# Kernel tuning notes

Measured on AMD Instinct MI355X. Metric: run time of the kernel, lower is better.

## Reference

```python
import jax, jax.numpy as jnp
import numpy as np

B, N, F, G, H = 8, 1024, 512, 128, 8
D = F // H  # head_dim = 64


def setup_inputs() -> dict:
    key = jax.random.key(0)
    ks = jax.random.split(key, 24)
    def lin(k, fan_in, shape):
        return jax.random.normal(k, shape, jnp.float32) / np.sqrt(fan_in)
    return {
        "features": jax.random.normal(ks[0], (B, N, F), jnp.float32),
        "geometry": jax.random.normal(ks[1], (B, N, G), jnp.float32),
        "coords": jax.random.normal(ks[2], (B, N, 3), jnp.float32),
        # nnx.MultiHeadAttention params (q/k/v/out dense, with bias)
        "wq": lin(ks[3], F, (F, F)), "bq": jnp.zeros((F,), jnp.float32),
        "wk": lin(ks[4], F, (F, F)), "bk": jnp.zeros((F,), jnp.float32),
        "wv": lin(ks[5], F, (F, F)), "bv": jnp.zeros((F,), jnp.float32),
        "wo": lin(ks[6], F, (F, F)), "bo": jnp.zeros((F,), jnp.float32),
        # geometry q/k/v linears
        "gq_w": lin(ks[7], G, (G, F)), "gq_b": jnp.zeros((F,), jnp.float32),
        "gk_w": lin(ks[8], G, (G, F)), "gk_b": jnp.zeros((F,), jnp.float32),
        "gv_w": lin(ks[9], G, (G, F)), "gv_b": jnp.zeros((F,), jnp.float32),
        # distance MLP: Linear(1->H), gelu, Linear(H->H)
        "d1_w": lin(ks[10], 1, (1, H)), "d1_b": jnp.zeros((H,), jnp.float32),
        "d2_w": lin(ks[11], H, (H, H)), "d2_b": jnp.zeros((H,), jnp.float32),
        # output projection
        "op_w": lin(ks[12], F, (F, F)), "op_b": jnp.zeros((F,), jnp.float32),
    }


def _forward(features, geometry, coords,
             wq, bq, wk, bk, wv, bv, wo, bo,
             gq_w, gq_b, gk_w, gk_b, gv_w, gv_b,
             d1_w, d1_b, d2_w, d2_b, op_w, op_b):
    scale = jnp.sqrt(jnp.float32(D))
    # --- standard multi-head self-attention branch (nnx.MultiHeadAttention) ---
    q = (features @ wq + bq).reshape(B, N, H, D)
    k = (features @ wk + bk).reshape(B, N, H, D)
    v = (features @ wv + bv).reshape(B, N, H, D)
    scores = jnp.einsum("bqhd,bkhd->bhqk", q, k) / scale
    attn = jax.nn.softmax(scores, axis=-1)
    feat_att = jnp.einsum("bhqk,bkhd->bqhd", attn, v).reshape(B, N, F)
    feat_att = feat_att @ wo + bo
    # --- geometry attention branch ---
    gq = geometry @ gq_w + gq_b
    gk = geometry @ gk_w + gk_b
    gv = geometry @ gv_w + gv_b
    g_scores = jnp.einsum("bqd,bkd->bqk", gq, gk) / scale
    # pairwise distances (B,N,N,1); clamp for sqrt-at-zero safety (diagonal)
    diff = coords[:, :, None, :] - coords[:, None, :, :]
    dist = jnp.sqrt(jnp.maximum(jnp.sum(diff * diff, -1, keepdims=True), 1e-12))
    dw = jax.nn.gelu(dist @ d1_w + d1_b) @ d2_w + d2_b  # (B,N,N,H)
    # transpose to (B,H,N,N) then mean over heads == mean over last axis
    g_scores = g_scores + jnp.mean(dw, axis=-1)
    g_attn = jax.nn.softmax(g_scores, axis=-1)
    geom_att = jnp.einsum("bqk,bkd->bqd", g_attn, gv)
    return (feat_att + geom_att) @ op_w + op_b


def reference(features, geometry, coords,
              wq, bq, wk, bk, wv, bv, wo, bo,
              gq_w, gq_b, gk_w, gk_b, gv_w, gv_b,
              d1_w, d1_b, d2_w, d2_b, op_w, op_b):
    return _forward(features, geometry, coords,
                    wq, bq, wk, bk, wv, bv, wo, bo,
                    gq_w, gq_b, gk_w, gk_b, gv_w, gv_b,
                    d1_w, d1_b, d2_w, d2_b, op_w, op_b)
```

## Files before the change

kernel.cpp:

```cpp
#include <hip/hip_runtime.h>

typedef __bf16 bf16_t;
typedef __bf16 bf16x8 __attribute__((ext_vector_type(8)));
typedef __bf16 bf16x4v __attribute__((ext_vector_type(4)));
typedef float f32x4 __attribute__((ext_vector_type(4)));

#define MFMA16(a, b, c) __builtin_amdgcn_mfma_f32_16x16x32_bf16((a), (b), (c), 0, 0, 0)

static constexpr int B_ = 8, N_ = 1024, F_ = 512, H_ = 8;
static constexpr int M_ = B_ * N_;
static constexpr float LOG2E = 1.4426950408889634f;

__device__ __forceinline__ void gl_lds16(const bf16_t* gsrc, bf16_t* ldst) {
  __builtin_amdgcn_global_load_lds(
      (const __attribute__((address_space(1))) void*)gsrc,
      (__attribute__((address_space(3))) void*)ldst, 16, 0, 0);
}

__device__ __forceinline__ float gelu_tanh(float u) {
  float g = 0.7978845608028654f * fmaf(0.044715f * u * u, u, u);
  float e = __expf(2.f * g);
  float t = 1.f - 2.f / (e + 1.f);
  return 0.5f * u * (1.f + t);
}

struct PrepArgs {
  const float *features, *geometry;
  const float *wq, *wk, *wv, *wo, *op_w;
  const float *gq_w, *gk_w, *gv_w;
  const float *bq, *bk, *bv, *gq_b, *gv_b;
  const float *d1w, *d1b, *d2w, *d2b;
  bf16_t *featBF, *geomBF, *gkwBF, *WqkvT, *GqvT, *WoT, *OpT;
  float *bqkv, *gqvb, *dlut;
};

static constexpr int PR_C0 = 4096;
static constexpr int PR_C1 = PR_C0 + 1024;
static constexpr int PR_GKC = PR_C1 + 64;
static constexpr int PR_WQ = PR_GKC + 256;
static constexpr int PR_WK = PR_WQ + 256;
static constexpr int PR_WV = PR_WK + 256;
static constexpr int PR_WO = PR_WV + 256;
static constexpr int PR_OP = PR_WO + 256;
static constexpr int PR_GQ = PR_OP + 64;
static constexpr int PR_GV = PR_GQ + 64;
static constexpr int PR_B1 = PR_GV + 6;
static constexpr int PR_B2 = PR_B1 + 4;
static constexpr int PR_LUT = PR_B2 + 16;
static constexpr int PR_TOTAL = PR_LUT;

__device__ __forceinline__ void prep_cast(const float* __restrict__ in,
                                          bf16_t* __restrict__ out, int blk) {
  int i = blk * 256 + threadIdx.x;
  float4 v = ((const float4*)in)[i];
  bf16x4v o;
  o[0] = (bf16_t)v.x; o[1] = (bf16_t)v.y; o[2] = (bf16_t)v.z; o[3] = (bf16_t)v.w;
  ((bf16x4v*)out)[i] = o;
}

__device__ __forceinline__ void prep_transpose(const float* __restrict__ W,
                                               bf16_t* __restrict__ Wt,
                                               int K, int N, int ldo, int idx,
                                               float (*t)[33]) {
  const int bx = idx & 15, by = idx >> 4;
  const int kb = by * 32, cb = bx * 32;
  const int tx = threadIdx.x & 31, ty = threadIdx.x >> 5;
#pragma unroll
  for (int i = 0; i < 4; ++i)
    t[ty * 4 + i][tx] = W[(long)(kb + ty * 4 + i) * N + cb + tx];
  __syncthreads();
#pragma unroll
  for (int i = 0; i < 4; ++i)
    Wt[(long)(cb + ty * 4 + i) * ldo + kb + tx] = (bf16_t)t[tx][ty * 4 + i];
}

__global__ __launch_bounds__(256) void k_prep(PrepArgs p) {
  __shared__ float tsh[32][33];
  const int blk = blockIdx.x;
  if (blk < PR_C0) {
    prep_cast(p.features, p.featBF, blk);
  } else if (blk < PR_C1) {
    prep_cast(p.geometry, p.geomBF, blk - PR_C0);
  } else if (blk < PR_GKC) {
    prep_cast(p.gk_w, p.gkwBF, blk - PR_C1);
  } else if (blk < PR_WQ) {
    prep_transpose(p.wq, p.WqkvT, 512, 512, 512, blk - PR_GKC, tsh);
  } else if (blk < PR_WK) {
    prep_transpose(p.wk, p.WqkvT + 512 * 512, 512, 512, 512, blk - PR_WQ, tsh);
  } else if (blk < PR_WV) {
    prep_transpose(p.wv, p.WqkvT + 1024 * 512, 512, 512, 512, blk - PR_WK, tsh);
  } else if (blk < PR_WO) {
    prep_transpose(p.wo, p.WoT, 512, 512, 512, blk - PR_WV, tsh);
  } else if (blk < PR_OP) {
    prep_transpose(p.op_w, p.OpT, 512, 512, 512, blk - PR_WO, tsh);
  } else if (blk < PR_GQ) {
    prep_transpose(p.gq_w, p.GqvT, 128, 512, 128, blk - PR_OP, tsh);
  } else if (blk < PR_GV) {
    prep_transpose(p.gv_w, p.GqvT + 512 * 128, 128, 512, 128, blk - PR_GQ, tsh);
  } else if (blk < PR_B1) {
    int i = (blk - PR_GV) * 256 + threadIdx.x;
    p.bqkv[i] = i < 512 ? p.bq[i] : (i < 1024 ? p.bk[i - 512] : p.bv[i - 1024]);
  } else if (blk < PR_B2) {
    int i = (blk - PR_B1) * 256 + threadIdx.x;
    p.gqvb[i] = i < 512 ? p.gq_b[i] : p.gv_b[i - 512];
  } else {
    int i = (blk - PR_B2) * 256 + threadIdx.x;
    float d = (i + 0.5f) * (16.f / 4096.f);
    float s = 0.f;
#pragma unroll
    for (int h = 0; h < 8; ++h) s += p.d2b[h];
    s *= 0.125f;
#pragma unroll
    for (int j = 0; j < 8; ++j) {
      float w2 = 0.f;
#pragma unroll
      for (int h = 0; h < 8; ++h) w2 += p.d2w[j * 8 + h];
      s = fmaf(gelu_tanh(fmaf(d, p.d1w[j], p.d1b[j])), w2 * 0.125f, s);
    }
    p.dlut[i] = s;
  }
}

struct GemmArgs {
  const bf16_t* A; const bf16_t* Bt;
  const float* bias; const float* addSrc; const bf16_t* addSrcB;
  const float* coords; const float* lut;
  float* outF; bf16_t* outB;
  bf16_t* outT;
  int vtileFrom;
  long strideAb; long strideBb;
  int lda, ldb, K, ldout;
  float scale;
};

__device__ __forceinline__ void gemm128_core(const GemmArgs& g, int mBase, int cBase,
                                             bf16_t (*As)[64], bf16_t (*Bs)[64]) {
  const int tid = threadIdx.x;
  const int w = tid >> 6, lane = tid & 63;
  const int lr = lane & 15, lg = lane >> 4;
  const int wr = w >> 1, wc = w & 1;
  const int batch = mBase >> 10;

  const int srow = lane >> 3;
  const int scol = (lane & 7) * 8;
  const bf16_t* Ag = g.A + (long)batch * g.strideAb +
                     (long)((mBase & 1023) + w * 32 + srow) * g.lda + scol;
  const bf16_t* Bg = g.Bt + (long)batch * g.strideBb +
                     (long)(cBase + w * 32 + srow) * g.ldb + scol;
  bf16_t* Al = &As[w * 32][0];
  bf16_t* Bl = &Bs[w * 32][0];

  f32x4 zero = {0.f, 0.f, 0.f, 0.f};
  f32x4 acc[4][4];
#pragma unroll
  for (int i = 0; i < 4; ++i)
#pragma unroll
    for (int j = 0; j < 4; ++j) acc[i][j] = zero;

  for (int k0 = 0; k0 < g.K; k0 += 64) {
#pragma unroll
    for (int is = 0; is < 4; ++is) {
      gl_lds16(Ag + (long)(is * 8) * g.lda + k0, Al + is * 8 * 64);
      gl_lds16(Bg + (long)(is * 8) * g.ldb + k0, Bl + is * 8 * 64);
    }
    __syncthreads();
#pragma unroll
    for (int ks = 0; ks < 2; ++ks) {
      bf16x8 a[4], b[4];
#pragma unroll
      for (int i = 0; i < 4; ++i) {
        a[i] = *(const bf16x8*)(&As[wr * 64 + i * 16 + lr][ks * 32 + lg * 8]);
        b[i] = *(const bf16x8*)(&Bs[wc * 64 + i * 16 + lr][ks * 32 + lg * 8]);
      }
#pragma unroll
      for (int mf = 0; mf < 4; ++mf)
#pragma unroll
        for (int nf = 0; nf < 4; ++nf)
          acc[mf][nf] = MFMA16(a[mf], b[nf], acc[mf][nf]);
    }
    __syncthreads();
  }

  const int c0 = cBase + wc * 64;
  float bias4[4];
#pragma unroll
  for (int nf = 0; nf < 4; ++nf)
    bias4[nf] = g.bias ? g.bias[c0 + nf * 16 + lr] : 0.f;
  const bool vtile = (g.outT != nullptr) && (cBase >= g.vtileFrom);
#pragma unroll
  for (int mf = 0; mf < 4; ++mf) {
    const int r0 = mBase + wr * 64 + mf * 16 + lg * 4;
    const int r0b = r0 & 1023;
#pragma unroll
    for (int nf = 0; nf < 4; ++nf) {
      const int c = c0 + nf * 16 + lr;
      if (vtile) {
        bf16x4v vv;
#pragma unroll
        for (int rg = 0; rg < 4; ++rg)
          vv[rg] = (bf16_t)(acc[mf][nf][rg] * g.scale + bias4[nf]);
        *(bf16x4v*)(&g.outT[((long)batch * 512 + (c - g.vtileFrom)) * 1024 + r0b]) = vv;
      } else {
#pragma unroll
        for (int rg = 0; rg < 4; ++rg) {
          const int r = r0 + rg;
          float v = acc[mf][nf][rg] * g.scale + bias4[nf];
          if (g.addSrc) v += g.addSrc[(long)r * g.ldout + c];
          const long oi = (long)r * g.ldout + c;
          if (g.outF) g.outF[oi] = v;
          if (g.outB) g.outB[oi] = (bf16_t)v;
        }
      }
    }
  }
}

__global__ __launch_bounds__(256) void k_gemm128_dual(GemmArgs g1, GemmArgs g2) {
  __shared__ alignas(16) bf16_t As[128][64];
  __shared__ alignas(16) bf16_t Bs[128][64];
  const int bx = blockIdx.x;
  if (bx < 768) {
    gemm128_core(g1, (bx / 12) * 128, (bx % 12) * 128, As, Bs);
  } else {
    const int i = bx - 768;
    gemm128_core(g2, (i / 8) * 128, (i % 8) * 128, As, Bs);
  }
}

__device__ __forceinline__ void gemm128_dist(const GemmArgs& g, int mBase, int cBase,
                                             char* smemc) {
  bf16_t (*As)[64] = (bf16_t (*)[64])smemc;
  bf16_t (*Bs)[64] = (bf16_t (*)[64])(smemc + 16384);
  bf16_t* Lut = (bf16_t*)(smemc + 32768);
  const int tid = threadIdx.x;
  const int w = tid >> 6, lane = tid & 63;
  const int lr = lane & 15, lg = lane >> 4;
  const int wr = w >> 1, wc = w & 1;
  const int batch = mBase >> 10;

  {
    const float4* src = (const float4*)g.lut;
#pragma unroll
    for (int i = 0; i < 4; ++i) {
      float4 v = src[tid + i * 256];
      bf16x4v o;
      o[0] = (bf16_t)(v.x * LOG2E); o[1] = (bf16_t)(v.y * LOG2E);
      o[2] = (bf16_t)(v.z * LOG2E); o[3] = (bf16_t)(v.w * LOG2E);
      ((bf16x4v*)Lut)[tid + i * 256] = o;
    }
  }

  const int srow = lane >> 3;
  const int scol = (lane & 7) * 8;
  const bf16_t* Ag = g.A + (long)batch * g.strideAb +
                     (long)((mBase & 1023) + w * 32 + srow) * g.lda + scol;
  const bf16_t* Bg = g.Bt + (long)batch * g.strideBb +
                     (long)(cBase + w * 32 + srow) * g.ldb + scol;
  bf16_t* Al = &As[w * 32][0];
  bf16_t* Bl = &Bs[w * 32][0];

  f32x4 zero = {0.f, 0.f, 0.f, 0.f};
  f32x4 acc[4][4];
#pragma unroll
  for (int i = 0; i < 4; ++i)
#pragma unroll
    for (int j = 0; j < 4; ++j) acc[i][j] = zero;

  for (int k0 = 0; k0 < g.K; k0 += 64) {
#pragma unroll
    for (int is = 0; is < 4; ++is) {
      gl_lds16(Ag + (long)(is * 8) * g.lda + k0, Al + is * 8 * 64);
      gl_lds16(Bg + (long)(is * 8) * g.ldb + k0, Bl + is * 8 * 64);
    }
    __syncthreads();
#pragma unroll
    for (int ks = 0; ks < 2; ++ks) {
      bf16x8 a[4], b[4];
#pragma unroll
      for (int i = 0; i < 4; ++i) {
        a[i] = *(const bf16x8*)(&As[wr * 64 + i * 16 + lr][ks * 32 + lg * 8]);
        b[i] = *(const bf16x8*)(&Bs[wc * 64 + i * 16 + lr][ks * 32 + lg * 8]);
      }
#pragma unroll
      for (int mf = 0; mf < 4; ++mf)
#pragma unroll
        for (int nf = 0; nf < 4; ++nf)
          acc[mf][nf] = MFMA16(a[mf], b[nf], acc[mf][nf]);
    }
    __syncthreads();
  }

  const int c0 = cBase + wc * 64;
  float ckx[4], cky[4], ckz[4];
#pragma unroll
  for (int nf = 0; nf < 4; ++nf) {
    const float* ck = g.coords + ((long)batch * 1024 + c0 + nf * 16 + lr) * 3;
    ckx[nf] = ck[0]; cky[nf] = ck[1]; ckz[nf] = ck[2];
  }
#pragma unroll
  for (int mf = 0; mf < 4; ++mf) {
    const int r0 = mBase + wr * 64 + mf * 16 + lg * 4;
    float cqx[4], cqy[4], cqz[4];
#pragma unroll
    for (int rg = 0; rg < 4; ++rg) {
      const float* cq = g.coords + ((long)batch * 1024 + ((r0 + rg) & 1023)) * 3;
      cqx[rg] = cq[0]; cqy[rg] = cq[1]; cqz[rg] = cq[2];
    }
#pragma unroll
    for (int nf = 0; nf < 4; ++nf) {
      const int c = c0 + nf * 16 + lr;
#pragma unroll
      for (int rg = 0; rg < 4; ++rg) {
        const int r = r0 + rg;
        float v = acc[mf][nf][rg] * g.scale;
        float dx = cqx[rg] - ckx[nf], dy = cqy[rg] - cky[nf], dz = cqz[rg] - ckz[nf];
        float d = sqrtf(fmaxf(dx * dx + dy * dy + dz * dz, 1e-12f));
        int idx = (int)(d * 256.f);
        idx = idx > 4095 ? 4095 : idx;
        g.outB[(long)r * g.ldout + c] = (bf16_t)exp2f(v + (float)Lut[idx]);
      }
    }
  }
}

__device__ __forceinline__ void flash_core(const bf16_t* __restrict__ QKV,
                                           const bf16_t* __restrict__ Vt,
                                           bf16_t* __restrict__ fatt,
                                           int qx, int bh, char* smemc) {
  bf16_t (*Ks)[64][64] = (bf16_t (*)[64][64])smemc;
  bf16_t (*Vs)[64][64] = (bf16_t (*)[64][64])(smemc + 16384);
  char* Plb = smemc + 32768;
  const int wave = threadIdx.x >> 6, lane = threadIdx.x & 63;
  const int lr = lane & 15, lg = (lane >> 4) & 3;
  const int b = bh >> 3, h = bh & 7;
  const int qbase = qx * 64 + wave * 16;

  const bf16_t* Qb = QKV + (long)b * 1024 * 1536 + h * 64;
  const bf16_t* Kb = Qb + 512;
  const bf16_t* Vg = Vt + ((long)b * 512 + h * 64) * 1024;

  constexpr float SCL = 0.18033688011112042f;
  bf16x8 q_[2];
#pragma unroll
  for (int dh = 0; dh < 2; ++dh) {
    bf16x8 raw = *(const bf16x8*)(Qb + (long)(qbase + lr) * 1536 + dh * 32 + lg * 8);
#pragma unroll
    for (int j = 0; j < 8; ++j) q_[dh][j] = (bf16_t)((float)raw[j] * SCL);
  }
  bf16x8 onesb;
#pragma unroll
  for (int j = 0; j < 8; ++j) onesb[j] = (bf16_t)1.0f;

  const int srow = lane >> 3;
  const int scol = (((lane & 7) ^ srow) << 3);
  const bf16_t* KgB = Kb + (long)(wave * 16 + srow) * 1536 + scol;
  const bf16_t* VgB = Vg + (long)(wave * 16 + srow) * 1024 + scol;

  auto stage = [&](int buf, int kt) {
#pragma unroll
    for (int i = 0; i < 2; ++i) {
      gl_lds16(KgB + (long)(kt + i * 8) * 1536, &Ks[buf][wave * 16 + i * 8][0]);
      gl_lds16(VgB + (long)(i * 8) * 1024 + kt, &Vs[buf][wave * 16 + i * 8][0]);
    }
  };

  f32x4 zero = {0.f, 0.f, 0.f, 0.f};
  f32x4 oacc[4] = {zero, zero, zero, zero};
  f32x4 oL = zero;
  const int swz = (lr & 7) << 4;
  char* PlW = Plb + wave * 1280;

  stage(0, 0);
  asm volatile("s_waitcnt vmcnt(0)" ::: "memory");
  __syncthreads();

  auto tile = [&](const int buf, int t) __attribute__((always_inline)) {
    if (t < 15) stage(buf ^ 1, (t + 1) * 64);
    const char* KB = (const char*)&Ks[buf][0][0];
    const char* VB = (const char*)&Vs[buf][0][0];
#pragma unroll
    for (int kk = 0; kk < 2; ++kk) {
      f32x4 S[2];
      __builtin_amdgcn_s_setprio(1);
#pragma unroll
      for (int kh = 0; kh < 2; ++kh) {
        const int row = kk * 32 + kh * 16 + lr;
        bf16x8 k0 = *(const bf16x8*)(KB + row * 128 + ((lg * 16) ^ swz));
        bf16x8 k1 = *(const bf16x8*)(KB + row * 128 + ((64 + lg * 16) ^ swz));
        f32x4 tt = MFMA16(k0, q_[0], zero);
        S[kh] = MFMA16(k1, q_[1], tt);
      }
      __builtin_amdgcn_s_setprio(0);
#pragma unroll
      for (int kh = 0; kh < 2; ++kh) {
        bf16x4v pp;
#pragma unroll
        for (int r = 0; r < 4; ++r) pp[r] = (bf16_t)exp2f(S[kh][r]);
        *(bf16x4v*)(PlW + lr * 80 + kh * 32 + lg * 8) = pp;
      }
      asm volatile("s_waitcnt lgkmcnt(0)" ::: "memory");
      const bf16x8 pa = *(const bf16x8*)(PlW + lr * 80 + lg * 16);
      __builtin_amdgcn_s_setprio(1);
#pragma unroll
      for (int ct = 0; ct < 4; ++ct) {
        const int vrow = ct * 16 + lr;
        bf16x8 vf = *(const bf16x8*)(VB + vrow * 128 + ((kk * 64 + lg * 16) ^ swz));
        oacc[ct] = MFMA16(pa, vf, oacc[ct]);
      }
      oL = MFMA16(pa, onesb, oL);
      __builtin_amdgcn_s_setprio(0);
    }
    asm volatile("s_waitcnt vmcnt(0)" ::: "memory");
    __syncthreads();
  };

  for (int tt = 0; tt < 8; ++tt) {
    tile(0, tt * 2);
    tile(1, tt * 2 + 1);
  }

#pragma unroll
  for (int r = 0; r < 4; ++r) {
    float inv = 1.f / oL[r];
    int q = qbase + lg * 4 + r;
    bf16_t* orow = fatt + ((long)b * 1024 + q) * 512 + h * 64;
#pragma unroll
    for (int ct = 0; ct < 4; ++ct)
      orow[ct * 16 + lr] = (bf16_t)(oacc[ct][r] * inv);
  }
}

__global__ __launch_bounds__(256) void k_gsc_flash(GemmArgs g,
                                                   const bf16_t* __restrict__ QKV,
                                                   const bf16_t* __restrict__ Vt,
                                                   bf16_t* __restrict__ fatt) {
  __shared__ alignas(16) char smem[40960];
  const int bx = blockIdx.x;
  if (bx < 512) {
    gemm128_dist(g, (bx >> 3) * 128, (bx & 7) * 128, smem);
  } else {
    const int fid = bx - 512;
    flash_core(QKV, Vt, fatt, fid & 15, fid >> 4, smem);
  }
}

template <int RSUM>
__global__ __launch_bounds__(256) void k_gemm_n64(GemmArgs g) {
  __shared__ alignas(16) bf16_t As[128][64];
  __shared__ alignas(16) bf16_t Bs[64][64];
  const int tid = threadIdx.x;
  const int w = tid >> 6, lane = tid & 63;
  const int lr = lane & 15, lg = lane >> 4;
  const int wr = w >> 1, wc = w & 1;
  const int mBase = blockIdx.y * 128, cBase = blockIdx.x * 64;
  const int batch = mBase >> 10;

  const int srow = lane >> 3;
  const int scol = (lane & 7) * 8;
  const bf16_t* Ag = g.A + (long)batch * g.strideAb +
                     (long)((mBase & 1023) + w * 32 + srow) * g.lda + scol;
  const bf16_t* Bg = g.Bt + (long)batch * g.strideBb +
                     (long)(cBase + w * 16 + srow) * g.ldb + scol;
  bf16_t* Al = &As[w * 32][0];
  bf16_t* Bl = &Bs[w * 16][0];

  f32x4 zero = {0.f, 0.f, 0.f, 0.f};
  f32x4 acc[4][2];
#pragma unroll
  for (int i = 0; i < 4; ++i)
#pragma unroll
    for (int j = 0; j < 2; ++j) acc[i][j] = zero;
  f32x4 lacc[4] = {zero, zero, zero, zero};
  bf16x8 onesb;
#pragma unroll
  for (int j = 0; j < 8; ++j) onesb[j] = (bf16_t)1.0f;

  for (int k0 = 0; k0 < g.K; k0 += 64) {
#pragma unroll
    for (int is = 0; is < 4; ++is)
      gl_lds16(Ag + (long)(is * 8) * g.lda + k0, Al + is * 8 * 64);
#pragma unroll
    for (int is = 0; is < 2; ++is)
      gl_lds16(Bg + (long)(is * 8) * g.ldb + k0, Bl + is * 8 * 64);
    __syncthreads();
#pragma unroll
    for (int ks = 0; ks < 2; ++ks) {
      bf16x8 a[4], b[2];
#pragma unroll
      for (int i = 0; i < 4; ++i)
        a[i] = *(const bf16x8*)(&As[wr * 64 + i * 16 + lr][ks * 32 + lg * 8]);
#pragma unroll
      for (int j = 0; j < 2; ++j)
        b[j] = *(const bf16x8*)(&Bs[wc * 32 + j * 16 + lr][ks * 32 + lg * 8]);
#pragma unroll
      for (int mf = 0; mf < 4; ++mf)
#pragma unroll
        for (int nf = 0; nf < 2; ++nf)
          acc[mf][nf] = MFMA16(a[mf], b[nf], acc[mf][nf]);
      if constexpr (RSUM) {
#pragma unroll
        for (int mf = 0; mf < 4; ++mf)
          lacc[mf] = MFMA16(a[mf], onesb, lacc[mf]);
      }
    }
    __syncthreads();
  }

  const int c0 = cBase + wc * 32;
  float bias2[2];
#pragma unroll
  for (int nf = 0; nf < 2; ++nf)
    bias2[nf] = g.bias ? g.bias[c0 + nf * 16 + lr] : 0.f;
#pragma unroll
  for (int mf = 0; mf < 4; ++mf) {
    const int r0 = mBase + wr * 64 + mf * 16 + lg * 4;
    float linv[4];
    if constexpr (RSUM) {
#pragma unroll
      for (int rg = 0; rg < 4; ++rg) linv[rg] = 1.f / lacc[mf][rg];
    }
#pragma unroll
    for (int nf = 0; nf < 2; ++nf) {
      const int c = c0 + nf * 16 + lr;
#pragma unroll
      for (int rg = 0; rg < 4; ++rg) {
        const int r = r0 + rg;
        float v = acc[mf][nf][rg] * g.scale + bias2[nf];
        if constexpr (RSUM) v *= linv[rg];
        const long oi = (long)r * g.ldout + c;
        if (g.addSrc) v += g.addSrc[oi];
        if (g.addSrcB) v += (float)g.addSrcB[oi];
        if (g.outF) g.outF[oi] = v;
        if (g.outB) g.outB[oi] = (bf16_t)v;
      }
    }
  }
}

extern "C" void kernel_launch(void* const* d_in, const int* in_sizes, int n_in,
                              void* d_out, int out_size, void* d_ws, size_t ws_size,
                              hipStream_t stream) {
  const float* features = (const float*)d_in[0];
  const float* geometry = (const float*)d_in[1];
  const float* coords   = (const float*)d_in[2];
  const float* wq = (const float*)d_in[3];  const float* bq = (const float*)d_in[4];
  const float* wk = (const float*)d_in[5];  const float* bk = (const float*)d_in[6];
  const float* wv = (const float*)d_in[7];  const float* bv = (const float*)d_in[8];
  const float* wo = (const float*)d_in[9];  const float* bo = (const float*)d_in[10];
  const float* gq_w = (const float*)d_in[11]; const float* gq_b = (const float*)d_in[12];
  const float* gk_w = (const float*)d_in[13]; const float* gk_b = (const float*)d_in[14];
  const float* gv_w = (const float*)d_in[15]; const float* gv_b = (const float*)d_in[16];
  const float* d1_w = (const float*)d_in[17]; const float* d1_b = (const float*)d_in[18];
  const float* d2_w = (const float*)d_in[19]; const float* d2_b = (const float*)d_in[20];
  const float* op_w = (const float*)d_in[21]; const float* op_b = (const float*)d_in[22];
  (void)gk_b;

  size_t off = 0;
  auto carve = [&](size_t bytes) {
    void* p = (char*)d_ws + off;
    off += (bytes + 255) & ~(size_t)255;
    return p;
  };
  bf16_t* featBF = (bf16_t*)carve((size_t)M_ * F_ * 2);
  bf16_t* geomBF = (bf16_t*)carve((size_t)M_ * 128 * 2);
  bf16_t* gkwBF  = (bf16_t*)carve((size_t)128 * 512 * 2);
  bf16_t* WqkvT  = (bf16_t*)carve((size_t)1536 * 512 * 2);
  bf16_t* GqvT   = (bf16_t*)carve((size_t)1024 * 128 * 2);
  bf16_t* WoT    = (bf16_t*)carve((size_t)512 * 512 * 2);
  bf16_t* OpT    = (bf16_t*)carve((size_t)512 * 512 * 2);
  float*  bqkv   = (float*)carve(1536 * 4);
  float*  gqvb   = (float*)carve(1024 * 4);
  float*  dlut   = (float*)carve(4096 * 4);
  bf16_t* QKV    = (bf16_t*)carve((size_t)M_ * 1536 * 2);
  bf16_t* GQV    = (bf16_t*)carve((size_t)M_ * 1024 * 2);
  bf16_t* GQeff  = (bf16_t*)carve((size_t)M_ * 128 * 2);
  bf16_t* Vt     = (bf16_t*)carve((size_t)B_ * 512 * 1024 * 2);
  bf16_t* GVt    = (bf16_t*)carve((size_t)B_ * 512 * 1024 * 2);
  bf16_t* Pun    = (bf16_t*)carve((size_t)M_ * 1024 * 2);
  bf16_t* fatt   = (bf16_t*)carve((size_t)M_ * 512 * 2);
  bf16_t* combFb = (bf16_t*)carve((size_t)M_ * 512 * 2);
  bf16_t* combB  = (bf16_t*)carve((size_t)M_ * 512 * 2);
  if (off > ws_size) return;

  PrepArgs p;
  p.features = features; p.geometry = geometry;
  p.wq = wq; p.wk = wk; p.wv = wv; p.wo = wo; p.op_w = op_w;
  p.gq_w = gq_w; p.gk_w = gk_w; p.gv_w = gv_w;
  p.bq = bq; p.bk = bk; p.bv = bv; p.gq_b = gq_b; p.gv_b = gv_b;
  p.d1w = d1_w; p.d1b = d1_b; p.d2w = d2_w; p.d2b = d2_b;
  p.featBF = featBF; p.geomBF = geomBF; p.gkwBF = gkwBF; p.WqkvT = WqkvT;
  p.GqvT = GqvT; p.WoT = WoT; p.OpT = OpT;
  p.bqkv = bqkv; p.gqvb = gqvb; p.dlut = dlut;
  k_prep<<<PR_TOTAL, 256, 0, stream>>>(p);

  auto mk = [](const bf16_t* A, long sAb, int lda, const bf16_t* Bt, long sBb, int ldb,
               int K, const float* bias, const float* addSrc, const bf16_t* addSrcB,
               float* outF, bf16_t* outB, int ldout, float scale,
               const float* coords, const float* lut, bf16_t* outT, int vtileFrom) {
    GemmArgs g;
    g.A = A; g.Bt = Bt; g.bias = bias; g.addSrc = addSrc; g.addSrcB = addSrcB;
    g.coords = coords; g.lut = lut; g.outF = outF; g.outB = outB; g.outT = outT;
    g.vtileFrom = vtileFrom;
    g.strideAb = sAb; g.strideBb = sBb; g.lda = lda; g.ldb = ldb;
    g.K = K; g.ldout = ldout; g.scale = scale;
    return g;
  };

  k_gemm128_dual<<<1280, 256, 0, stream>>>(
      mk(featBF, (long)1024 * 512, 512, WqkvT, 0, 512, 512,
         bqkv, nullptr, nullptr, nullptr, QKV, 1536, 1.f, nullptr, nullptr, Vt, 1024),
      mk(geomBF, (long)1024 * 128, 128, GqvT, 0, 128, 128,
         gqvb, nullptr, nullptr, nullptr, GQV, 1024, 1.f, nullptr, nullptr, GVt, 512));
  k_gemm_n64<0><<<dim3(2, 64), 256, 0, stream>>>(
      mk(GQV, (long)1024 * 1024, 1024, gkwBF, 0, 512, 512,
         nullptr, nullptr, nullptr, nullptr, GQeff, 128, 1.f, nullptr, nullptr,
         nullptr, 1 << 30));
  k_gsc_flash<<<1536, 256, 0, stream>>>(
      mk(GQeff, (long)1024 * 128, 128, geomBF, (long)1024 * 128, 128, 128,
         nullptr, nullptr, nullptr, nullptr, Pun, 1024, 0.125f * LOG2E,
         coords, dlut, nullptr, 1 << 30),
      QKV, Vt, fatt);
  k_gemm_n64<0><<<dim3(8, 64), 256, 0, stream>>>(
      mk(fatt, (long)1024 * 512, 512, WoT, 0, 512, 512,
         bo, nullptr, nullptr, nullptr, combFb, 512, 1.f, nullptr, nullptr,
         nullptr, 1 << 30));
  k_gemm_n64<1><<<dim3(8, 64), 256, 0, stream>>>(
      mk(Pun, (long)1024 * 1024, 1024, GVt, (long)512 * 1024, 1024, 1024,
         nullptr, nullptr, combFb, nullptr, combB, 512, 1.f, nullptr, nullptr,
         nullptr, 1 << 30));
  k_gemm_n64<0><<<dim3(8, 64), 256, 0, stream>>>(
      mk(combB, (long)1024 * 512, 512, OpT, 0, 512, 512,
         op_b, nullptr, nullptr, (float*)d_out, nullptr, 512, 1.f, nullptr, nullptr,
         nullptr, 1 << 30));
}
```

Before: 184.4 us.

## Fuse Wo projection and geometry PV GEMM into one kernel, shrink tiles to 64x64

The out-projection GEMM (fatt@Wo+bo) and the normalized geometry attention GEMM (Pun@GVt with row-sum) now run in one kernel. It accumulates both products in registers and writes only the combined bf16 result, so the combFb intermediate round-trip and one launch go away. All n64 GEMMs also drop from 128x64 to 64x64 tiles, doubling the block count to fill more CUs on the small-N GEMMs. The cost is more total operand reloads per output and less MFMA reuse per LDS load.

```diff
diff --git a/kernel.cpp b/kernel.cpp
--- a/kernel.cpp
+++ b/kernel.cpp
@@ -445,66 +445,70 @@
 }
 
 template <int RSUM>
-__global__ __launch_bounds__(256) void k_gemm_n64(GemmArgs g) {
-  __shared__ alignas(16) bf16_t As[128][64];
+__device__ __forceinline__ void m64_loop(const GemmArgs& g, int mBase, int cBase,
+                                         bf16_t (*As)[64], bf16_t (*Bs)[64],
+                                         f32x4 (*acc)[2], f32x4* lacc) {
+  const int tid = threadIdx.x;
+  const int w = tid >> 6, lane = tid & 63;
+  const int lr = lane & 15, lg = lane >> 4;
+  const int wr = w >> 1, wc = w & 1;
+  const int batch = mBase >> 10;
+
+  const int srow = lane >> 3;
+  const int scol = (lane & 7) * 8;
+  const bf16_t* Ag = g.A + (long)batch * g.strideAb +
+                     (long)((mBase & 1023) + w * 16 + srow) * g.lda + scol;
+  const bf16_t* Bg = g.Bt + (long)batch * g.strideBb +
+                     (long)(cBase + w * 16 + srow) * g.ldb + scol;
+  bf16_t* Al = &As[w * 16][0];
+  bf16_t* Bl = &Bs[w * 16][0];
+
+  bf16x8 onesb;
+#pragma unroll
+  for (int j = 0; j < 8; ++j) onesb[j] = (bf16_t)1.0f;
+
+  for (int k0 = 0; k0 < g.K; k0 += 64) {
+#pragma unroll
+    for (int is = 0; is < 2; ++is) {
+      gl_lds16(Ag + (long)(is * 8) * g.lda + k0, Al + is * 8 * 64);
+      gl_lds16(Bg + (long)(is * 8) * g.ldb + k0, Bl + is * 8 * 64);
+    }
+    __syncthreads();
+#pragma unroll
+    for (int ks = 0; ks < 2; ++ks) {
+      bf16x8 a[2], b[2];
+#pragma unroll
+      for (int i = 0; i < 2; ++i) {
+        a[i] = *(const bf16x8*)(&As[wr * 32 + i * 16 + lr][ks * 32 + lg * 8]);
+        b[i] = *(const bf16x8*)(&Bs[wc * 32 + i * 16 + lr][ks * 32 + lg * 8]);
+      }
+#pragma unroll
+      for (int mf = 0; mf < 2; ++mf)
+#pragma unroll
+        for (int nf = 0; nf < 2; ++nf)
+          acc[mf][nf] = MFMA16(a[mf], b[nf], acc[mf][nf]);
+      if constexpr (RSUM) {
+#pragma unroll
+        for (int mf = 0; mf < 2; ++mf)
+          lacc[mf] = MFMA16(a[mf], onesb, lacc[mf]);
+      }
+    }
+    __syncthreads();
+  }
+}
+
+__global__ __launch_bounds__(256) void k_gemm_m64(GemmArgs g) {
+  __shared__ alignas(16) bf16_t As[64][64];
   __shared__ alignas(16) bf16_t Bs[64][64];
   const int tid = threadIdx.x;
   const int w = tid >> 6, lane = tid & 63;
   const int lr = lane & 15, lg = lane >> 4;
   const int wr = w >> 1, wc = w & 1;
-  const int mBase = blockIdx.y * 128, cBase = blockIdx.x * 64;
-  const int batch = mBase >> 10;
-
-  const int srow = lane >> 3;
-  const int scol = (lane & 7) * 8;
-  const bf16_t* Ag = g.A + (long)batch * g.strideAb +
-                     (long)((mBase & 1023) + w * 32 + srow) * g.lda + scol;
-  const bf16_t* Bg = g.Bt + (long)batch * g.strideBb +
-                     (long)(cBase + w * 16 + srow) * g.ldb + scol;
-  bf16_t* Al = &As[w * 32][0];
-  bf16_t* Bl = &Bs[w * 16][0];
+  const int mBase = blockIdx.y * 64, cBase = blockIdx.x * 64;
 
   f32x4 zero = {0.f, 0.f, 0.f, 0.f};
-  f32x4 acc[4][2];
-#pragma unroll
-  for (int i = 0; i < 4; ++i)
-#pragma unroll
-    for (int j = 0; j < 2; ++j) acc[i][j] = zero;
-  f32x4 lacc[4] = {zero, zero, zero, zero};
-  bf16x8 onesb;
-#pragma unroll
-  for (int j = 0; j < 8; ++j) onesb[j] = (bf16_t)1.0f;
-
-  for (int k0 = 0; k0 < g.K; k0 += 64) {
-#pragma unroll
-    for (int is = 0; is < 4; ++is)
-      gl_lds16(Ag + (long)(is * 8) * g.lda + k0, Al + is * 8 * 64);
-#pragma unroll
-    for (int is = 0; is < 2; ++is)
-      gl_lds16(Bg + (long)(is * 8) * g.ldb + k0, Bl + is * 8 * 64);
-    __syncthreads();
-#pragma unroll
-    for (int ks = 0; ks < 2; ++ks) {
-      bf16x8 a[4], b[2];
-#pragma unroll
-      for (int i = 0; i < 4; ++i)
-        a[i] = *(const bf16x8*)(&As[wr * 64 + i * 16 + lr][ks * 32 + lg * 8]);
-#pragma unroll
-      for (int j = 0; j < 2; ++j)
-        b[j] = *(const bf16x8*)(&Bs[wc * 32 + j * 16 + lr][ks * 32 + lg * 8]);
-#pragma unroll
-      for (int mf = 0; mf < 4; ++mf)
-#pragma unroll
-        for (int nf = 0; nf < 2; ++nf)
-          acc[mf][nf] = MFMA16(a[mf], b[nf], acc[mf][nf]);
-      if constexpr (RSUM) {
-#pragma unroll
-        for (int mf = 0; mf < 4; ++mf)
-          lacc[mf] = MFMA16(a[mf], onesb, lacc[mf]);
-      }
-    }
-    __syncthreads();
-  }
+  f32x4 acc[2][2] = {{zero, zero}, {zero, zero}};
+  m64_loop<0>(g, mBase, cBase, As, Bs, acc, nullptr);
 
   const int c0 = cBase + wc * 32;
   float bias2[2];
@@ -512,13 +516,8 @@
   for (int nf = 0; nf < 2; ++nf)
     bias2[nf] = g.bias ? g.bias[c0 + nf * 16 + lr] : 0.f;
 #pragma unroll
-  for (int mf = 0; mf < 4; ++mf) {
-    const int r0 = mBase + wr * 64 + mf * 16 + lg * 4;
-    float linv[4];
-    if constexpr (RSUM) {
-#pragma unroll
-      for (int rg = 0; rg < 4; ++rg) linv[rg] = 1.f / lacc[mf][rg];
-    }
+  for (int mf = 0; mf < 2; ++mf) {
+    const int r0 = mBase + wr * 32 + mf * 16 + lg * 4;
 #pragma unroll
     for (int nf = 0; nf < 2; ++nf) {
       const int c = c0 + nf * 16 + lr;
@@ -526,12 +525,50 @@
       for (int rg = 0; rg < 4; ++rg) {
         const int r = r0 + rg;
         float v = acc[mf][nf][rg] * g.scale + bias2[nf];
-        if constexpr (RSUM) v *= linv[rg];
         const long oi = (long)r * g.ldout + c;
-        if (g.addSrc) v += g.addSrc[oi];
-        if (g.addSrcB) v += (float)g.addSrcB[oi];
         if (g.outF) g.outF[oi] = v;
         if (g.outB) g.outB[oi] = (bf16_t)v;
+      }
+    }
+  }
+}
+
+__global__ __launch_bounds__(256) void k_comb(GemmArgs gF, GemmArgs gG,
+                                              bf16_t* __restrict__ outB) {
+  __shared__ alignas(16) bf16_t As[64][64];
+  __shared__ alignas(16) bf16_t Bs[64][64];
+  const int tid = threadIdx.x;
+  const int w = tid >> 6, lane = tid & 63;
+  const int lr = lane & 15, lg = lane >> 4;
+  const int wr = w >> 1, wc = w & 1;
+  const int mBase = blockIdx.y * 64, cBase = blockIdx.x * 64;
+
+  f32x4 zero = {0.f, 0.f, 0.f, 0.f};
+  f32x4 acc1[2][2] = {{zero, zero}, {zero, zero}};
+  f32x4 acc2[2][2] = {{zero, zero}, {zero, zero}};
+  f32x4 lacc[2] = {zero, zero};
+  m64_loop<0>(gF, mBase, cBase, As, Bs, acc1, nullptr);
+  m64_loop<1>(gG, mBase, cBase, As, Bs, acc2, lacc);
+
+  const int c0 = cBase + wc * 32;
+  float bias2[2];
+#pragma unroll
+  for (int nf = 0; nf < 2; ++nf)
+    bias2[nf] = gF.bias[c0 + nf * 16 + lr];
+#pragma unroll
+  for (int mf = 0; mf < 2; ++mf) {
+    const int r0 = mBase + wr * 32 + mf * 16 + lg * 4;
+    float linv[4];
+#pragma unroll
+    for (int rg = 0; rg < 4; ++rg) linv[rg] = 1.f / lacc[mf][rg];
+#pragma unroll
+    for (int nf = 0; nf < 2; ++nf) {
+      const int c = c0 + nf * 16 + lr;
+#pragma unroll
+      for (int rg = 0; rg < 4; ++rg) {
+        const int r = r0 + rg;
+        float v = acc2[mf][nf][rg] * linv[rg] + acc1[mf][nf][rg] + bias2[nf];
+        outB[(long)r * 512 + c] = (bf16_t)v;
       }
     }
   }
@@ -578,7 +615,6 @@
   bf16_t* GVt    = (bf16_t*)carve((size_t)B_ * 512 * 1024 * 2);
   bf16_t* Pun    = (bf16_t*)carve((size_t)M_ * 1024 * 2);
   bf16_t* fatt   = (bf16_t*)carve((size_t)M_ * 512 * 2);
-  bf16_t* combFb = (bf16_t*)carve((size_t)M_ * 512 * 2);
   bf16_t* combB  = (bf16_t*)carve((size_t)M_ * 512 * 2);
   if (off > ws_size) return;
 
@@ -611,7 +647,7 @@
          bqkv, nullptr, nullptr, nullptr, QKV, 1536, 1.f, nullptr, nullptr, Vt, 1024),
       mk(geomBF, (long)1024 * 128, 128, GqvT, 0, 128, 128,
          gqvb, nullptr, nullptr, nullptr, GQV, 1024, 1.f, nullptr, nullptr, GVt, 512));
-  k_gemm_n64<0><<<dim3(2, 64), 256, 0, stream>>>(
+  k_gemm_m64<<<dim3(2, 128), 256, 0, stream>>>(
       mk(GQV, (long)1024 * 1024, 1024, gkwBF, 0, 512, 512,
          nullptr, nullptr, nullptr, nullptr, GQeff, 128, 1.f, nullptr, nullptr,
          nullptr, 1 << 30));
@@ -620,15 +656,15 @@
          nullptr, nullptr, nullptr, nullptr, Pun, 1024, 0.125f * LOG2E,
          coords, dlut, nullptr, 1 << 30),
       QKV, Vt, fatt);
-  k_gemm_n64<0><<<dim3(8, 64), 256, 0, stream>>>(
+  k_comb<<<dim3(8, 128), 256, 0, stream>>>(
       mk(fatt, (long)1024 * 512, 512, WoT, 0, 512, 512,
-         bo, nullptr, nullptr, nullptr, combFb, 512, 1.f, nullptr, nullptr,
-         nullptr, 1 << 30));
-  k_gemm_n64<1><<<dim3(8, 64), 256, 0, stream>>>(
+         bo, nullptr, nullptr, nullptr, nullptr, 512, 1.f, nullptr, nullptr,
+         nullptr, 1 << 30),
       mk(Pun, (long)1024 * 1024, 1024, GVt, (long)512 * 1024, 1024, 1024,
-         nullptr, nullptr, combFb, nullptr, combB, 512, 1.f, nullptr, nullptr,
-         nullptr, 1 << 30));
-  k_gemm_n64<0><<<dim3(8, 64), 256, 0, stream>>>(
+         nullptr, nullptr, nullptr, nullptr, nullptr, 512, 1.f, nullptr, nullptr,
+         nullptr, 1 << 30),
+      combB);
+  k_gemm_m64<<<dim3(8, 128), 256, 0, stream>>>(
       mk(combB, (long)1024 * 512, 512, OpT, 0, 512, 512,
          op_b, nullptr, nullptr, (float*)d_out, nullptr, 512, 1.f, nullptr, nullptr,
          nullptr, 1 << 30));
```

After: 166.7 us. 1.11x faster.
